# Optimization experiments

Hardware: AMD Instinct MI355X
Metric: run time of the kernel (lower is better)

## Reference

```python
import jax, jax.numpy as jnp
import numpy as np
from jax import lax

INPUT_SIZE = 16
HIDDEN = 32
CHANNELS = 12
LP_NORM = 2.0
POOL_K = 3
POOL_S = 2
# nn.RReLU in eval mode uses the fixed slope (lower+upper)/2 for negative inputs
RRELU_SLOPE = (0.125 + 0.333) / 2.0


def setup_inputs() -> dict:
    key = jax.random.key(0)
    ks = jax.random.split(key, 8)
    x = jax.random.normal(ks[0], (4096, 2048, INPUT_SIZE), dtype=jnp.float32)
    bound_rnn = 1.0 / np.sqrt(HIDDEN)
    W_ih = jax.random.uniform(ks[1], (HIDDEN, INPUT_SIZE), jnp.float32, -bound_rnn, bound_rnn)
    W_hh = jax.random.uniform(ks[2], (HIDDEN, HIDDEN), jnp.float32, -bound_rnn, bound_rnn)
    b_ih = jax.random.uniform(ks[3], (HIDDEN,), jnp.float32, -bound_rnn, bound_rnn)
    b_hh = jax.random.uniform(ks[4], (HIDDEN,), jnp.float32, -bound_rnn, bound_rnn)
    bound_p = 1.0 / np.sqrt(HIDDEN)
    W_proj = jax.random.uniform(ks[5], (CHANNELS, HIDDEN), jnp.float32, -bound_p, bound_p)
    b_proj = jax.random.uniform(ks[6], (CHANNELS,), jnp.float32, -bound_p, bound_p)
    return {"x": x, "W_ih": W_ih, "W_hh": W_hh, "b_ih": b_ih, "b_hh": b_hh,
            "W_proj": W_proj, "b_proj": b_proj}


def reference(x, W_ih, W_hh, b_ih, b_hh, W_proj, b_proj):
    B, T, F = x.shape
    h0 = jnp.zeros((B, HIDDEN), dtype=x.dtype)

    def step(h, xt):
        # RNNCell (tanh); note the *pre-RReLU* hidden state is carried forward
        h_new = jnp.tanh(xt @ W_ih.T + b_ih + h @ W_hh.T + b_hh)
        h_act = jnp.where(h_new >= 0, h_new, h_new * RRELU_SLOPE)  # eval-mode RReLU
        p = h_act @ W_proj.T + b_proj  # (B, C)
        return h_new, p

    _, ps = lax.scan(step, h0, jnp.transpose(x, (1, 0, 2)))  # ps: (T, B, C)
    stacked = jnp.transpose(ps, (1, 2, 0))  # (B, C, T)

    # LPPool1d with p=2: (sum over window of x^p)^(1/p)
    powed = stacked * stacked
    summed = lax.reduce_window(powed, 0.0, lax.add,
                               window_dimensions=(1, 1, POOL_K),
                               window_strides=(1, 1, POOL_S),
                               padding=((0, 0), (0, 0), (0, 0)))
    pooled = jnp.sqrt(summed)  # (B, C, L_out)
    return jnp.max(pooled, axis=1)  # (B, L_out)
```

## Files before the change

### kernel.cpp

```cpp
#include <hip/hip_runtime.h>
#include <math.h>

#define T_LEN   2048
#define B_ROWS  4096
#define F_IN    16
#define HID     32
#define NCH     12
#define L_OUT   1023
#define TCH     16
#define NCHUNK  (T_LEN / TCH)
#define RRELU_SLOPE 0.229f
#define ZSCALE  2.8853900817779268f

typedef _Float16 half4 __attribute__((ext_vector_type(4)));
typedef _Float16 half8 __attribute__((ext_vector_type(8)));
typedef float    f32x4 __attribute__((ext_vector_type(4)));

__device__ __forceinline__ f32x4 mfma16(half4 a, half4 b, f32x4 c) {
    return __builtin_amdgcn_mfma_f32_16x16x16f16(a, b, c, 0, 0, 0);
}

__device__ __forceinline__ f32x4 hmfma32(half8 a, half8 b, f32x4 c) {
#if __has_builtin(__builtin_amdgcn_mfma_f32_16x16x32_f16)
    return __builtin_amdgcn_mfma_f32_16x16x32_f16(a, b, c, 0, 0, 0);
#else
    const uint4 ua = __builtin_bit_cast(uint4, a);
    const uint4 ub = __builtin_bit_cast(uint4, b);
    uint2 t;
    t.x = ua.x; t.y = ua.y; const half4 alo = __builtin_bit_cast(half4, t);
    t.x = ua.z; t.y = ua.w; const half4 ahi = __builtin_bit_cast(half4, t);
    t.x = ub.x; t.y = ub.y; const half4 blo = __builtin_bit_cast(half4, t);
    t.x = ub.z; t.y = ub.w; const half4 bhi = __builtin_bit_cast(half4, t);
    return mfma16(ahi, bhi, mfma16(alo, blo, c));
#endif
}

__device__ __forceinline__ float act_fast(float zs) {
    float e = __builtin_amdgcn_exp2f(zs);
    float r = __builtin_amdgcn_rcpf(e + 1.0f);
    return fmaf(-2.0f, r, 1.0f);
}

__device__ __forceinline__ unsigned pk2u(float a, float b) {
    return __builtin_bit_cast(unsigned, __builtin_amdgcn_cvt_pkrtz(a, b));
}
__device__ __forceinline__ half4 pack4(float a, float b, float c, float d) {
    uint2 u; u.x = pk2u(a, b); u.y = pk2u(c, d);
    return __builtin_bit_cast(half4, u);
}

__device__ __forceinline__ uint4 u4(f32x4 v) { return __builtin_bit_cast(uint4, v); }
__device__ __forceinline__ f32x4 f4(uint4 v) { return __builtin_bit_cast(f32x4, v); }

__global__ __launch_bounds__(192, 1)
void rnn_mfma_kernel(const float* __restrict__ x,
                     const float* __restrict__ W_ih,
                     const float* __restrict__ W_hh,
                     const float* __restrict__ b_ih,
                     const float* __restrict__ b_hh,
                     const float* __restrict__ W_proj,
                     const float* __restrict__ b_proj,
                     float* __restrict__ out)
{
    __shared__ alignas(16) uint4 hqs[2][TCH][64];
    __shared__ alignas(16) uint4 xza_s[2][TCH][64];
    __shared__ alignas(16) uint4 xzb_s[2][TCH][64];
    __shared__ alignas(16) float pbuf[64];

    const int tid  = threadIdx.x;
    const int wid  = tid >> 6;
    const int lane = tid & 63;
    const int c16  = lane & 15;
    const int g    = lane >> 4;
    const int rowBase = blockIdx.x * 16;

    const f32x4 zero4 = {0.0f, 0.0f, 0.0f, 0.0f};

    const float4* xsrc = (const float4*)x;
    const size_t xrow = (size_t)(rowBase + c16) * T_LEN;
    float* outrow = out + (size_t)(rowBase + c16) * L_OUT;

    half8 AhhF[2];
    half4 Aih[2];
    half8 ApF;
    f32x4 biasA = zero4, biasB = zero4, biasP = zero4;
    float4 xsA[TCH], xsB[TCH];

    if (wid == 0) {
        #pragma unroll
        for (int U = 0; U < 2; ++U) {
            half8 f;
            #pragma unroll
            for (int V = 0; V < 2; ++V)
                #pragma unroll
                for (int i = 0; i < 4; ++i)
                    f[V*4 + i] = (_Float16)(ZSCALE *
                        W_hh[(U*16 + c16)*HID + V*16 + 4*g + i]);
            AhhF[U] = f;
        }
    } else if (wid == 1) {
        #pragma unroll
        for (int U = 0; U < 2; ++U)
            #pragma unroll
            for (int i = 0; i < 4; ++i)
                Aih[U][i] = (_Float16)(ZSCALE *
                    W_ih[(U*16 + c16)*F_IN + 4*g + i]);
        #pragma unroll
        for (int r = 0; r < 4; ++r) {
            const int u = 4*g + r;
            biasA[r] = ZSCALE * (b_ih[u]      + b_hh[u]);
            biasB[r] = ZSCALE * (b_ih[16 + u] + b_hh[16 + u]);
        }
    } else {
        #pragma unroll
        for (int V = 0; V < 2; ++V)
            #pragma unroll
            for (int i = 0; i < 4; ++i)
                ApF[V*4 + i] = (c16 < NCH)
                    ? (_Float16)W_proj[c16*HID + V*16 + 4*g + i]
                    : (_Float16)0.0f;
        #pragma unroll
        for (int r = 0; r < 4; ++r) {
            const int u = 4*g + r;
            biasP[r] = (u < NCH) ? b_proj[u] : 0.0f;
        }
    }

    half8 Bh = {0,0,0,0,0,0,0,0};
    f32x4 Wc = zero4;

    auto w1_load = [&](int c, float4* xs) {
        const int cc = (c < NCHUNK) ? c : NCHUNK - 1;
        #pragma unroll
        for (int m = 0; m < TCH; ++m)
            xs[m] = xsrc[(xrow + cc*TCH + m) * 4 + g];
    };
    auto w1_compute = [&](int buf, const float4* xs) {
        #pragma unroll
        for (int m = 0; m < TCH; ++m) {
            const half4 Bx = pack4(xs[m].x, xs[m].y, xs[m].z, xs[m].w);
            xza_s[buf][m][lane] = u4(mfma16(Aih[0], Bx, biasA));
            xzb_s[buf][m][lane] = u4(mfma16(Aih[1], Bx, biasB));
        }
    };

    auto w0_chunk = [&](int buf) {
        uint4 ra[4], rb[4];
        #pragma unroll
        for (int i = 0; i < 4; ++i) {
            ra[i] = xza_s[buf][i][lane];
            rb[i] = xzb_s[buf][i][lane];
        }
        #pragma unroll
        for (int tt = 0; tt < TCH; ++tt) {
            const f32x4 xza = f4(ra[tt & 3]);
            const f32x4 xzb = f4(rb[tt & 3]);
            const f32x4 za = hmfma32(AhhF[0], Bh, xza);
            const f32x4 zb = hmfma32(AhhF[1], Bh, xzb);
            if (tt + 4 < TCH) {
                ra[tt & 3] = xza_s[buf][tt + 4][lane];
                rb[tt & 3] = xzb_s[buf][tt + 4][lane];
            }
            uint4 hp;
            hp.x = pk2u(act_fast(za[0]), act_fast(za[1]));
            hp.y = pk2u(act_fast(za[2]), act_fast(za[3]));
            hp.z = pk2u(act_fast(zb[0]), act_fast(zb[1]));
            hp.w = pk2u(act_fast(zb[2]), act_fast(zb[3]));
            Bh = __builtin_bit_cast(half8, hp);
            hqs[buf][tt][lane] = hp;
        }
    };

    const half8 sl8 = {(_Float16)RRELU_SLOPE, (_Float16)RRELU_SLOPE,
                       (_Float16)RRELU_SLOPE, (_Float16)RRELU_SLOPE,
                       (_Float16)RRELU_SLOPE, (_Float16)RRELU_SLOPE,
                       (_Float16)RRELU_SLOPE, (_Float16)RRELU_SLOPE};
    auto w2_process = [&](int c, int buf) {
        #pragma unroll
        for (int tt = 0; tt < TCH; ++tt) {
            const int t = c*TCH + tt;
            const uint4 hv = hqs[buf][tt][lane];
            const half8 h8 = __builtin_bit_cast(half8, hv);
            const half8 a8 = __builtin_elementwise_max(h8, h8 * sl8);
            const f32x4 p  = hmfma32(ApF, a8, biasP);
            const f32x4 q4 = p * p;
            if ((tt & 1) == 0) {
                const f32x4 pr = Wc + q4;
                if (t >= 2) {
                    const float mloc = fmaxf(fmaxf(pr[0], pr[1]),
                                             fmaxf(pr[2], pr[3]));
                    pbuf[c16*4 + g] = mloc;
                    if (g == 0) {
                        const f32x4 pv = *(const f32x4*)&pbuf[c16*4];
                        const float mm = fmaxf(fmaxf(pv[0], pv[1]),
                                               fmaxf(pv[2], pv[3]));
                        outrow[(t >> 1) - 1] = __builtin_amdgcn_sqrtf(mm);
                    }
                }
                Wc = q4;
            } else {
                Wc = Wc + q4;
            }
        }
    };

    if (wid == 1) {
        w1_load(0, xsA);
        w1_compute(0, xsA);
        w1_load(1, xsA);
    }
    __syncthreads();

    for (int cc = 0; cc < NCHUNK; cc += 2) {
        if (wid == 0) {
            w0_chunk(0);
        } else if (wid == 1) {
            w1_load(cc + 2, xsB);
            w1_compute(1, xsA);
        } else {
            if (cc > 0) w2_process(cc - 1, 1);
        }
        __syncthreads();
        if (wid == 0) {
            w0_chunk(1);
        } else if (wid == 1) {
            w1_load(cc + 3, xsA);
            w1_compute(0, xsB);
        } else {
            w2_process(cc, 0);
        }
        __syncthreads();
    }
    if (wid == 2) w2_process(NCHUNK - 1, 1);
}

extern "C" void kernel_launch(void* const* d_in, const int* in_sizes, int n_in,
                              void* d_out, int out_size, void* d_ws, size_t ws_size,
                              hipStream_t stream) {
    const float* x      = (const float*)d_in[0];
    const float* W_ih   = (const float*)d_in[1];
    const float* W_hh   = (const float*)d_in[2];
    const float* b_ih   = (const float*)d_in[3];
    const float* b_hh   = (const float*)d_in[4];
    const float* W_proj = (const float*)d_in[5];
    const float* b_proj = (const float*)d_in[6];
    float* out = (float*)d_out;

    dim3 grid(B_ROWS / 16);
    dim3 block(192);
    hipLaunchKernelGGL(rnn_mfma_kernel, grid, block, 0, stream,
                       x, W_ih, W_hh, b_ih, b_hh, W_proj, b_proj, out);
}
```

Baseline: 309.4 us.

## Interleave two independent 16-row recurrences per block, halve chunk length

Each block now handles 32 batch rows as two independent 16-row groups. The recurrence wave interleaves the two MFMA chains to hide the dependent MFMA and tanh latency of the serial recurrence. The two support waves each own one group, doing both the input projection and the output projection/pooling, and the chunk length drops from 16 to 8 timesteps. The grid is halved to 128 blocks, so fewer CUs are used (MI355X has 256). Barrier frequency doubles because of the shorter chunks.

```diff
diff --git a/kernel.cpp b/kernel.cpp
--- a/kernel.cpp
+++ b/kernel.cpp
@@ -7,7 +7,7 @@
 #define HID     32
 #define NCH     12
 #define L_OUT   1023
-#define TCH     16
+#define TCH     8
 #define NCHUNK  (T_LEN / TCH)
 #define RRELU_SLOPE 0.229f
 #define ZSCALE  2.8853900817779268f
@@ -62,29 +62,36 @@
                      const float* __restrict__ b_proj,
                      float* __restrict__ out)
 {
-    __shared__ alignas(16) uint4 hqs[2][TCH][64];
-    __shared__ alignas(16) uint4 xza_s[2][TCH][64];
-    __shared__ alignas(16) uint4 xzb_s[2][TCH][64];
-    __shared__ alignas(16) float pbuf[64];
+    __shared__ alignas(16) uint4 hqs[2][2][TCH][64];
+    __shared__ alignas(16) uint4 xza_s[2][2][TCH][64];
+    __shared__ alignas(16) uint4 xzb_s[2][2][TCH][64];
+    __shared__ alignas(16) float pbuf[2][64];
 
     const int tid  = threadIdx.x;
     const int wid  = tid >> 6;
     const int lane = tid & 63;
     const int c16  = lane & 15;
     const int g    = lane >> 4;
-    const int rowBase = blockIdx.x * 16;
+    const int rowBase = blockIdx.x * 32;
 
     const f32x4 zero4 = {0.0f, 0.0f, 0.0f, 0.0f};
-
     const float4* xsrc = (const float4*)x;
-    const size_t xrow = (size_t)(rowBase + c16) * T_LEN;
-    float* outrow = out + (size_t)(rowBase + c16) * L_OUT;
 
     half8 AhhF[2];
+    half8 Bh0 = {0,0,0,0,0,0,0,0}, Bh1 = {0,0,0,0,0,0,0,0};
+
+    const int ci = (wid > 0) ? (wid - 1) : 0;
+    const size_t xrow = (size_t)(rowBase + ci*16 + c16) * T_LEN;
+    float* outrow = out + (size_t)(rowBase + ci*16 + c16) * L_OUT;
     half4 Aih[2];
     half8 ApF;
     f32x4 biasA = zero4, biasB = zero4, biasP = zero4;
     float4 xsA[TCH], xsB[TCH];
+    const half8 sl8 = {(_Float16)RRELU_SLOPE, (_Float16)RRELU_SLOPE,
+                       (_Float16)RRELU_SLOPE, (_Float16)RRELU_SLOPE,
+                       (_Float16)RRELU_SLOPE, (_Float16)RRELU_SLOPE,
+                       (_Float16)RRELU_SLOPE, (_Float16)RRELU_SLOPE};
+    f32x4 Wc = zero4;
 
     if (wid == 0) {
         #pragma unroll
@@ -98,20 +105,13 @@
                         W_hh[(U*16 + c16)*HID + V*16 + 4*g + i]);
             AhhF[U] = f;
         }
-    } else if (wid == 1) {
+    } else {
         #pragma unroll
         for (int U = 0; U < 2; ++U)
             #pragma unroll
             for (int i = 0; i < 4; ++i)
                 Aih[U][i] = (_Float16)(ZSCALE *
                     W_ih[(U*16 + c16)*F_IN + 4*g + i]);
-        #pragma unroll
-        for (int r = 0; r < 4; ++r) {
-            const int u = 4*g + r;
-            biasA[r] = ZSCALE * (b_ih[u]      + b_hh[u]);
-            biasB[r] = ZSCALE * (b_ih[16 + u] + b_hh[16 + u]);
-        }
-    } else {
         #pragma unroll
         for (int V = 0; V < 2; ++V)
             #pragma unroll
@@ -122,64 +122,66 @@
         #pragma unroll
         for (int r = 0; r < 4; ++r) {
             const int u = 4*g + r;
+            biasA[r] = ZSCALE * (b_ih[u]      + b_hh[u]);
+            biasB[r] = ZSCALE * (b_ih[16 + u] + b_hh[16 + u]);
             biasP[r] = (u < NCH) ? b_proj[u] : 0.0f;
         }
     }
 
-    half8 Bh = {0,0,0,0,0,0,0,0};
-    f32x4 Wc = zero4;
-
-    auto w1_load = [&](int c, float4* xs) {
+    auto w0_chunk = [&](int buf) {
+        uint4 ra0[2], rb0[2], ra1[2], rb1[2];
+        #pragma unroll
+        for (int i = 0; i < 2; ++i) {
+            ra0[i] = xza_s[0][buf][i][lane]; rb0[i] = xzb_s[0][buf][i][lane];
+            ra1[i] = xza_s[1][buf][i][lane]; rb1[i] = xzb_s[1][buf][i][lane];
+        }
+        #pragma unroll
+        for (int tt = 0; tt < TCH; ++tt) {
+            const f32x4 za0 = hmfma32(AhhF[0], Bh0, f4(ra0[tt & 1]));
+            const f32x4 zb0 = hmfma32(AhhF[1], Bh0, f4(rb0[tt & 1]));
+            const f32x4 za1 = hmfma32(AhhF[0], Bh1, f4(ra1[tt & 1]));
+            const f32x4 zb1 = hmfma32(AhhF[1], Bh1, f4(rb1[tt & 1]));
+            if (tt + 2 < TCH) {
+                ra0[tt & 1] = xza_s[0][buf][tt + 2][lane];
+                rb0[tt & 1] = xzb_s[0][buf][tt + 2][lane];
+                ra1[tt & 1] = xza_s[1][buf][tt + 2][lane];
+                rb1[tt & 1] = xzb_s[1][buf][tt + 2][lane];
+            }
+            uint4 hp0, hp1;
+            hp0.x = pk2u(act_fast(za0[0]), act_fast(za0[1]));
+            hp0.y = pk2u(act_fast(za0[2]), act_fast(za0[3]));
+            hp0.z = pk2u(act_fast(zb0[0]), act_fast(zb0[1]));
+            hp0.w = pk2u(act_fast(zb0[2]), act_fast(zb0[3]));
+            hp1.x = pk2u(act_fast(za1[0]), act_fast(za1[1]));
+            hp1.y = pk2u(act_fast(za1[2]), act_fast(za1[3]));
+            hp1.z = pk2u(act_fast(zb1[0]), act_fast(zb1[1]));
+            hp1.w = pk2u(act_fast(zb1[2]), act_fast(zb1[3]));
+            Bh0 = __builtin_bit_cast(half8, hp0);
+            Bh1 = __builtin_bit_cast(half8, hp1);
+            hqs[0][buf][tt][lane] = hp0;
+            hqs[1][buf][tt][lane] = hp1;
+        }
+    };
+
+    auto sup_load = [&](int c, float4* xs) {
         const int cc = (c < NCHUNK) ? c : NCHUNK - 1;
         #pragma unroll
         for (int m = 0; m < TCH; ++m)
             xs[m] = xsrc[(xrow + cc*TCH + m) * 4 + g];
     };
-    auto w1_compute = [&](int buf, const float4* xs) {
+    auto sup_xz = [&](int buf, const float4* xs) {
         #pragma unroll
         for (int m = 0; m < TCH; ++m) {
             const half4 Bx = pack4(xs[m].x, xs[m].y, xs[m].z, xs[m].w);
-            xza_s[buf][m][lane] = u4(mfma16(Aih[0], Bx, biasA));
-            xzb_s[buf][m][lane] = u4(mfma16(Aih[1], Bx, biasB));
-        }
-    };
-
-    auto w0_chunk = [&](int buf) {
-        uint4 ra[4], rb[4];
-        #pragma unroll
-        for (int i = 0; i < 4; ++i) {
-            ra[i] = xza_s[buf][i][lane];
-            rb[i] = xzb_s[buf][i][lane];
-        }
-        #pragma unroll
-        for (int tt = 0; tt < TCH; ++tt) {
-            const f32x4 xza = f4(ra[tt & 3]);
-            const f32x4 xzb = f4(rb[tt & 3]);
-            const f32x4 za = hmfma32(AhhF[0], Bh, xza);
-            const f32x4 zb = hmfma32(AhhF[1], Bh, xzb);
-            if (tt + 4 < TCH) {
-                ra[tt & 3] = xza_s[buf][tt + 4][lane];
-                rb[tt & 3] = xzb_s[buf][tt + 4][lane];
-            }
-            uint4 hp;
-            hp.x = pk2u(act_fast(za[0]), act_fast(za[1]));
-            hp.y = pk2u(act_fast(za[2]), act_fast(za[3]));
-            hp.z = pk2u(act_fast(zb[0]), act_fast(zb[1]));
-            hp.w = pk2u(act_fast(zb[2]), act_fast(zb[3]));
-            Bh = __builtin_bit_cast(half8, hp);
-            hqs[buf][tt][lane] = hp;
-        }
-    };
-
-    const half8 sl8 = {(_Float16)RRELU_SLOPE, (_Float16)RRELU_SLOPE,
-                       (_Float16)RRELU_SLOPE, (_Float16)RRELU_SLOPE,
-                       (_Float16)RRELU_SLOPE, (_Float16)RRELU_SLOPE,
-                       (_Float16)RRELU_SLOPE, (_Float16)RRELU_SLOPE};
-    auto w2_process = [&](int c, int buf) {
+            xza_s[ci][buf][m][lane] = u4(mfma16(Aih[0], Bx, biasA));
+            xzb_s[ci][buf][m][lane] = u4(mfma16(Aih[1], Bx, biasB));
+        }
+    };
+    auto sup_proj = [&](int c, int buf) {
         #pragma unroll
         for (int tt = 0; tt < TCH; ++tt) {
             const int t = c*TCH + tt;
-            const uint4 hv = hqs[buf][tt][lane];
+            const uint4 hv = hqs[ci][buf][tt][lane];
             const half8 h8 = __builtin_bit_cast(half8, hv);
             const half8 a8 = __builtin_elementwise_max(h8, h8 * sl8);
             const f32x4 p  = hmfma32(ApF, a8, biasP);
@@ -189,9 +191,9 @@
                 if (t >= 2) {
                     const float mloc = fmaxf(fmaxf(pr[0], pr[1]),
                                              fmaxf(pr[2], pr[3]));
-                    pbuf[c16*4 + g] = mloc;
+                    pbuf[ci][c16*4 + g] = mloc;
                     if (g == 0) {
-                        const f32x4 pv = *(const f32x4*)&pbuf[c16*4];
+                        const f32x4 pv = *(const f32x4*)&pbuf[ci][c16*4];
                         const float mm = fmaxf(fmaxf(pv[0], pv[1]),
                                                fmaxf(pv[2], pv[3]));
                         outrow[(t >> 1) - 1] = __builtin_amdgcn_sqrtf(mm);
@@ -204,34 +206,32 @@
         }
     };
 
-    if (wid == 1) {
-        w1_load(0, xsA);
-        w1_compute(0, xsA);
-        w1_load(1, xsA);
+    if (wid >= 1) {
+        sup_load(0, xsA);
+        sup_xz(0, xsA);
+        sup_load(1, xsA);
     }
     __syncthreads();
 
     for (int cc = 0; cc < NCHUNK; cc += 2) {
         if (wid == 0) {
             w0_chunk(0);
-        } else if (wid == 1) {
-            w1_load(cc + 2, xsB);
-            w1_compute(1, xsA);
         } else {
-            if (cc > 0) w2_process(cc - 1, 1);
+            sup_load(cc + 2, xsB);
+            sup_xz(1, xsA);
+            if (cc > 0) sup_proj(cc - 1, 1);
         }
         __syncthreads();
         if (wid == 0) {
             w0_chunk(1);
-        } else if (wid == 1) {
-            w1_load(cc + 3, xsA);
-            w1_compute(0, xsB);
         } else {
-            w2_process(cc, 0);
+            sup_load(cc + 3, xsA);
+            sup_xz(0, xsB);
+            sup_proj(cc, 0);
         }
         __syncthreads();
     }
-    if (wid == 2) w2_process(NCHUNK - 1, 1);
+    if (wid >= 1) sup_proj(NCHUNK - 1, 1);
 }
 
 extern "C" void kernel_launch(void* const* d_in, const int* in_sizes, int n_in,
@@ -246,7 +246,7 @@
     const float* b_proj = (const float*)d_in[6];
     float* out = (float*)d_out;
 
-    dim3 grid(B_ROWS / 16);
+    dim3 grid(B_ROWS / 32);
     dim3 block(192);
     hipLaunchKernelGGL(rnn_mfma_kernel, grid, block, 0, stream,
                        x, W_ih, W_hh, b_ih, b_hh, W_proj, b_proj, out);
```

Result: slower. 564.6 us (+82.5%).
